# Kernel tuning notes

Hardware: AMD Instinct MI355X
Metric: run time of the kernel (lower is better)

## Reference

```python
import jax, jax.numpy as jnp
import numpy as np

B, L, C = 4, 1024, 768
H = 12
D = C // H  # head_dim = 64


def setup_inputs() -> dict:
    key = jax.random.key(0)
    k_x, k_qkv, k_pw, k_pb = jax.random.split(key, 4)
    x = jax.random.normal(k_x, (B, L, C), dtype=jnp.float32)
    # torch nn.Linear(C, 3C, bias=False): weight [3C, C]
    w_qkv = jax.random.normal(k_qkv, (3 * C, C), dtype=jnp.float32) * (1.0 / np.sqrt(C))
    # torch nn.Linear(C, C): weight [C, C], bias [C]
    w_proj = jax.random.normal(k_pw, (C, C), dtype=jnp.float32) * (1.0 / np.sqrt(C))
    b_proj = jax.random.normal(k_pb, (C,), dtype=jnp.float32) * 0.01
    return {"x": x, "w_qkv": w_qkv, "w_proj": w_proj, "b_proj": b_proj}


def reference(x, w_qkv, w_proj, b_proj):
    scale = D ** (-0.5)
    # qkv: [B, L, 3C] -> [3, B, H, L, D]
    qkv = jnp.einsum('blc,fc->blf', x, w_qkv)
    qkv = qkv.reshape(B, L, 3, H, D).transpose(2, 0, 3, 1, 4)
    q, k, v = qkv[0], qkv[1], qkv[2]
    # attention scores [B, H, L, L], materialized (returned by the module)
    attn = jnp.einsum('bhld,bhmd->bhlm', q, k) * scale
    attn_score = jax.nn.softmax(attn, axis=-1)
    # dropout_p = 0.0 -> identity
    out = jnp.einsum('bhlm,bhmd->bhld', attn_score, v)
    out = out.transpose(0, 2, 1, 3).reshape(B, L, C)
    out = jnp.einsum('blc,fc->blf', out, w_proj) + b_proj
    return (out, attn_score)
```

## Files before the change

kernel.cpp:

```cpp
#include <hip/hip_runtime.h>
#include <hip/hip_bf16.h>
#include <stdint.h>


typedef __attribute__((ext_vector_type(8))) short short8;
typedef __attribute__((ext_vector_type(4))) float floatx4;

#define MFMA16(A_, B_, C_) __builtin_amdgcn_mfma_f32_16x16x32_bf16((A_), (B_), (C_), 0, 0, 0)

__device__ __forceinline__ unsigned short f2bf(float f) {
  unsigned u = __builtin_bit_cast(unsigned, f);
  u += 0x7FFFu + ((u >> 16) & 1u);
  return (unsigned short)(u >> 16);
}
__device__ __forceinline__ float bf2f(unsigned short u) {
  return __builtin_bit_cast(float, (unsigned)u << 16);
}

__global__ __launch_bounds__(256) void cast3_kernel(const float* __restrict__ x,
                                                    const float* __restrict__ wq,
                                                    const float* __restrict__ wp,
                                                    unsigned short* __restrict__ dst) {
  const int NX = 3145728, NWQ = 1769472;
  int i = (blockIdx.x * 256 + threadIdx.x) * 4;
  const float* src;
  int off;
  if (i < NX) { src = x; off = i; }
  else if (i < NX + NWQ) { src = wq; off = i - NX; }
  else { src = wp; off = i - NX - NWQ; }
  float4 v = *(const float4*)(src + off);
  ushort4 o;
  o.x = f2bf(v.x); o.y = f2bf(v.y); o.z = f2bf(v.z); o.w = f2bf(v.w);
  *(ushort4*)(dst + i) = o;
}

template <int EPI>
__global__ __launch_bounds__(256) void gemm_bt(
    const unsigned short* __restrict__ A, const unsigned short* __restrict__ Bm,
    const float* __restrict__ bias,
    unsigned short* __restrict__ q_ws, unsigned short* __restrict__ k_ws,
    unsigned short* __restrict__ vt_ws, float* __restrict__ Cout,
    int M, int N, int K) {
  __shared__ __align__(16) unsigned short Al[128 * 32];
  __shared__ __align__(16) unsigned short Bl[128 * 32];
  const int tid = threadIdx.x;
  const int lane = tid & 63, wave = tid >> 6;
  const int q = lane >> 4, lm = lane & 15;
  const int wm = wave >> 1, wn = wave & 1;
  const int m0 = blockIdx.y * 128, n0 = blockIdx.x * 128;

  floatx4 acc[4][4];
#pragma unroll
  for (int i = 0; i < 4; ++i)
#pragma unroll
    for (int j = 0; j < 4; ++j) acc[i][j] = (floatx4){0.f, 0.f, 0.f, 0.f};

  for (int k0 = 0; k0 < K; k0 += 32) {
#pragma unroll
    for (int it = 0; it < 2; ++it) {
      int idx = tid + it * 256;
      int row = idx >> 2, ch = idx & 3;
      const unsigned short* ga = A + (size_t)(m0 + row) * K + k0 + ch * 8;
      const unsigned short* gb = Bm + (size_t)(n0 + row) * K + k0 + ch * 8;
      __builtin_amdgcn_global_load_lds(
          (const __attribute__((address_space(1))) unsigned int*)ga,
          (__attribute__((address_space(3))) unsigned int*)(Al + idx * 8), 16, 0, 0);
      __builtin_amdgcn_global_load_lds(
          (const __attribute__((address_space(1))) unsigned int*)gb,
          (__attribute__((address_space(3))) unsigned int*)(Bl + idx * 8), 16, 0, 0);
    }
    __syncthreads();
    short8 af[4], bfr[4];
#pragma unroll
    for (int t = 0; t < 4; ++t) {
      af[t] = *(const short8*)(Al + (wm * 64 + t * 16 + lm) * 32 + q * 8);
      bfr[t] = *(const short8*)(Bl + (wn * 64 + t * 16 + lm) * 32 + q * 8);
    }
#pragma unroll
    for (int i = 0; i < 4; ++i)
#pragma unroll
      for (int j = 0; j < 4; ++j) acc[i][j] = MFMA16(af[i], bfr[j], acc[i][j]);
    __syncthreads();
  }

  if (EPI == 0) {
#pragma unroll
    for (int i = 0; i < 4; ++i) {
      int mb = m0 + wm * 64 + i * 16 + q * 4;
#pragma unroll
      for (int j = 0; j < 4; ++j) {
        int n = n0 + wn * 64 + j * 16 + lm;
        int which = n / 768;
        int r = n - which * 768;
        int h = r >> 6, d = r & 63;
        if (which == 2) {
          int b = mb >> 10, l = mb & 1023;
          ushort4 pk;
          pk.x = f2bf(acc[i][j][0]);
          pk.y = f2bf(acc[i][j][1]);
          pk.z = f2bf(acc[i][j][2]);
          pk.w = f2bf(acc[i][j][3]);
          *(ushort4*)(vt_ws + (size_t)((b * 12 + h) * 64 + d) * 1024 + l) = pk;
        } else {
          unsigned short* dst = (which == 0) ? q_ws : k_ws;
          float sc = (which == 0) ? 0.125f : 1.0f;
#pragma unroll
          for (int rg = 0; rg < 4; ++rg) {
            int m = mb + rg;
            int b = m >> 10, l = m & 1023;
            dst[(size_t)((b * 12 + h) * 1024 + l) * 64 + d] = f2bf(acc[i][j][rg] * sc);
          }
        }
      }
    }
  } else {
#pragma unroll
    for (int i = 0; i < 4; ++i) {
      int mb = m0 + wm * 64 + i * 16 + q * 4;
#pragma unroll
      for (int j = 0; j < 4; ++j) {
        int n = n0 + wn * 64 + j * 16 + lm;
        float bv = bias[n];
#pragma unroll
        for (int rg = 0; rg < 4; ++rg) {
          int m = mb + rg;
          Cout[(size_t)m * N + n] = acc[i][j][rg] + bv;
        }
      }
    }
  }
}

__global__ __launch_bounds__(256) void attn_mfma(
    const unsigned short* __restrict__ q_ws, const unsigned short* __restrict__ k_ws,
    const unsigned short* __restrict__ vt_ws, unsigned short* __restrict__ attn_o,
    float* __restrict__ out1) {
  constexpr int L = 1024, SW = 1032;
  __shared__ __align__(16) unsigned short S[16 * SW];
  __shared__ float stats[2][4][16];
  const int bh = blockIdx.y, b = bh / 12, h = bh % 12;
  const int l0 = blockIdx.x * 16;
  const int tid = threadIdx.x, lane = tid & 63, wave = tid >> 6;
  const int q = lane >> 4, lm = lane & 15;

  const size_t qk_base = (size_t)bh * L * 64;

  const unsigned short* qr = q_ws + qk_base + (size_t)(l0 + lm) * 64;
  short8 bq0 = *(const short8*)(qr + q * 8);
  short8 bq1 = *(const short8*)(qr + 32 + q * 8);

  floatx4 acc[16];
#pragma unroll
  for (int ct = 0; ct < 16; ++ct) {
    const unsigned short* kr = k_ws + qk_base + (size_t)((wave * 16 + ct) * 16 + lm) * 64;
    short8 a0 = *(const short8*)(kr + q * 8);
    short8 a1 = *(const short8*)(kr + 32 + q * 8);
    floatx4 c = (floatx4){0.f, 0.f, 0.f, 0.f};
    c = MFMA16(a0, bq0, c);
    c = MFMA16(a1, bq1, c);
    acc[ct] = c;
  }

  float mloc = -1e30f;
#pragma unroll
  for (int ct = 0; ct < 16; ++ct)
#pragma unroll
    for (int rg = 0; rg < 4; ++rg) mloc = fmaxf(mloc, acc[ct][rg]);
  mloc = fmaxf(mloc, __shfl_xor(mloc, 16));
  mloc = fmaxf(mloc, __shfl_xor(mloc, 32));
  if (lane < 16) stats[0][wave][lane] = mloc;
  __syncthreads();
  float m = fmaxf(fmaxf(stats[0][0][lm], stats[0][1][lm]),
                  fmaxf(stats[0][2][lm], stats[0][3][lm]));

  float ssum = 0.f;
#pragma unroll
  for (int ct = 0; ct < 16; ++ct) {
#pragma unroll
    for (int rg = 0; rg < 4; ++rg) {
      float e = exp2f((acc[ct][rg] - m) * 1.44269504f);
      acc[ct][rg] = e;
      ssum += e;
    }
  }
  ssum += __shfl_xor(ssum, 16);
  ssum += __shfl_xor(ssum, 32);
  if (lane < 16) stats[1][wave][lane] = ssum;
  __syncthreads();
  float sinv = 1.0f / (stats[1][0][lm] + stats[1][1][lm] + stats[1][2][lm] + stats[1][3][lm]);

  float* orow = out1 + (size_t)bh * L * L + (size_t)(l0 + lm) * L + wave * 256 + q * 4;
  unsigned short* srow = S + lm * SW + wave * 256 + q * 4;
#pragma unroll
  for (int ct = 0; ct < 16; ++ct) {
    float p0 = acc[ct][0] * sinv, p1 = acc[ct][1] * sinv;
    float p2 = acc[ct][2] * sinv, p3 = acc[ct][3] * sinv;
    ushort4 pk;
    pk.x = f2bf(p0); pk.y = f2bf(p1); pk.z = f2bf(p2); pk.w = f2bf(p3);
    *(ushort4*)(srow + ct * 16) = pk;
    float4 pv;
    pv.x = p0; pv.y = p1; pv.z = p2; pv.w = p3;
    *(float4*)(orow + ct * 16) = pv;
  }
  __syncthreads();

  {
    floatx4 pacc = (floatx4){0.f, 0.f, 0.f, 0.f};
    const unsigned short* vr = vt_ws + (size_t)(bh * 64 + wave * 16 + lm) * 1024;
#pragma unroll 4
    for (int ks = 0; ks < 32; ++ks) {
      short8 af = *(const short8*)(S + lm * SW + ks * 32 + q * 8);
      short8 bv = *(const short8*)(vr + ks * 32 + q * 8);
      pacc = MFMA16(af, bv, pacc);
    }
#pragma unroll
    for (int rg = 0; rg < 4; ++rg) {
      int row = q * 4 + rg;
      attn_o[(size_t)(b * 1024 + l0 + row) * 768 + h * 64 + wave * 16 + lm] = f2bf(pacc[rg]);
    }
  }
}

extern "C" void kernel_launch(void* const* d_in, const int* in_sizes, int n_in,
                              void* d_out, int out_size, void* d_ws, size_t ws_size,
                              hipStream_t stream) {
  const float* x      = (const float*)d_in[0];
  const float* w_qkv  = (const float*)d_in[1];
  const float* w_proj = (const float*)d_in[2];
  const float* b_proj = (const float*)d_in[3];

  float* out0 = (float*)d_out;
  float* out1 = out0 + (size_t)4096 * 768;

  const size_t NX = (size_t)4096 * 768;
  const size_t NWQ = (size_t)2304 * 768;
  const size_t NWP = (size_t)768 * 768;
  const size_t NQ = (size_t)48 * 1024 * 64;

  unsigned short* x_bf   = (unsigned short*)d_ws;
  unsigned short* wq_bf  = x_bf + NX;
  unsigned short* wp_bf  = wq_bf + NWQ;
  unsigned short* q_ws   = wp_bf + NWP;
  unsigned short* k_ws   = q_ws + NQ;
  unsigned short* vt_ws  = k_ws + NQ;
  unsigned short* attn_o = vt_ws + NQ;

  cast3_kernel<<<dim3((NX + NWQ + NWP) / 1024), dim3(256), 0, stream>>>(x, w_qkv, w_proj, x_bf);

  gemm_bt<0><<<dim3(2304 / 128, 4096 / 128), dim3(256), 0, stream>>>(
      x_bf, wq_bf, nullptr, q_ws, k_ws, vt_ws, nullptr, 4096, 2304, 768);

  attn_mfma<<<dim3(64, 48), dim3(256), 0, stream>>>(q_ws, k_ws, vt_ws, attn_o, out1);

  gemm_bt<1><<<dim3(768 / 128, 4096 / 128), dim3(256), 0, stream>>>(
      attn_o, wp_bf, b_proj, nullptr, nullptr, nullptr, out0, 4096, 768, 768);
}
```

Before: 359.3 us.

## Double-buffer GEMM LDS tiles and use narrower N tile for output projection

Measured after the change: 357.2 us. About the same (-0.6%).

```diff
diff --git a/kernel.cpp b/kernel.cpp
--- a/kernel.cpp
+++ b/kernel.cpp
@@ -34,53 +34,68 @@
   *(ushort4*)(dst + i) = o;
 }
 
-template <int EPI>
+template <int EPI, int BN>
 __global__ __launch_bounds__(256) void gemm_bt(
     const unsigned short* __restrict__ A, const unsigned short* __restrict__ Bm,
     const float* __restrict__ bias,
     unsigned short* __restrict__ q_ws, unsigned short* __restrict__ k_ws,
     unsigned short* __restrict__ vt_ws, float* __restrict__ Cout,
     int M, int N, int K) {
-  __shared__ __align__(16) unsigned short Al[128 * 32];
-  __shared__ __align__(16) unsigned short Bl[128 * 32];
+  constexpr int NJ = BN / 32;
+  constexpr int QN = BN / 2;
+  __shared__ __align__(16) unsigned short Al[2][128 * 32];
+  __shared__ __align__(16) unsigned short Bl[2][BN * 32];
   const int tid = threadIdx.x;
   const int lane = tid & 63, wave = tid >> 6;
   const int q = lane >> 4, lm = lane & 15;
   const int wm = wave >> 1, wn = wave & 1;
-  const int m0 = blockIdx.y * 128, n0 = blockIdx.x * 128;
-
-  floatx4 acc[4][4];
+  const int m0 = blockIdx.y * 128, n0 = blockIdx.x * BN;
+
+  floatx4 acc[4][NJ];
 #pragma unroll
   for (int i = 0; i < 4; ++i)
 #pragma unroll
-    for (int j = 0; j < 4; ++j) acc[i][j] = (floatx4){0.f, 0.f, 0.f, 0.f};
-
-  for (int k0 = 0; k0 < K; k0 += 32) {
+    for (int j = 0; j < NJ; ++j) acc[i][j] = (floatx4){0.f, 0.f, 0.f, 0.f};
+
+  auto stage = [&](int k0, int buf) {
 #pragma unroll
     for (int it = 0; it < 2; ++it) {
       int idx = tid + it * 256;
       int row = idx >> 2, ch = idx & 3;
       const unsigned short* ga = A + (size_t)(m0 + row) * K + k0 + ch * 8;
+      __builtin_amdgcn_global_load_lds(
+          (const __attribute__((address_space(1))) unsigned int*)ga,
+          (__attribute__((address_space(3))) unsigned int*)(&Al[buf][0] + idx * 8), 16, 0, 0);
+    }
+#pragma unroll
+    for (int it = 0; it < BN / 64; ++it) {
+      int idx = tid + it * 256;
+      int row = idx >> 2, ch = idx & 3;
       const unsigned short* gb = Bm + (size_t)(n0 + row) * K + k0 + ch * 8;
       __builtin_amdgcn_global_load_lds(
-          (const __attribute__((address_space(1))) unsigned int*)ga,
-          (__attribute__((address_space(3))) unsigned int*)(Al + idx * 8), 16, 0, 0);
-      __builtin_amdgcn_global_load_lds(
           (const __attribute__((address_space(1))) unsigned int*)gb,
-          (__attribute__((address_space(3))) unsigned int*)(Bl + idx * 8), 16, 0, 0);
-    }
+          (__attribute__((address_space(3))) unsigned int*)(&Bl[buf][0] + idx * 8), 16, 0, 0);
+    }
+  };
+
+  stage(0, 0);
+  __syncthreads();
+  int cur = 0;
+  for (int k0 = 0; k0 < K; k0 += 32) {
+    if (k0 + 32 < K) stage(k0 + 32, cur ^ 1);
+    short8 af[4], bfr[NJ];
+#pragma unroll
+    for (int t = 0; t < 4; ++t)
+      af[t] = *(const short8*)(&Al[cur][0] + (wm * 64 + t * 16 + lm) * 32 + q * 8);
+#pragma unroll
+    for (int t = 0; t < NJ; ++t)
+      bfr[t] = *(const short8*)(&Bl[cur][0] + (wn * QN + t * 16 + lm) * 32 + q * 8);
+#pragma unroll
+    for (int i = 0; i < 4; ++i)
+#pragma unroll
+      for (int j = 0; j < NJ; ++j) acc[i][j] = MFMA16(af[i], bfr[j], acc[i][j]);
     __syncthreads();
-    short8 af[4], bfr[4];
-#pragma unroll
-    for (int t = 0; t < 4; ++t) {
-      af[t] = *(const short8*)(Al + (wm * 64 + t * 16 + lm) * 32 + q * 8);
-      bfr[t] = *(const short8*)(Bl + (wn * 64 + t * 16 + lm) * 32 + q * 8);
-    }
-#pragma unroll
-    for (int i = 0; i < 4; ++i)
-#pragma unroll
-      for (int j = 0; j < 4; ++j) acc[i][j] = MFMA16(af[i], bfr[j], acc[i][j]);
-    __syncthreads();
+    cur ^= 1;
   }
 
   if (EPI == 0) {
@@ -88,8 +103,8 @@
     for (int i = 0; i < 4; ++i) {
       int mb = m0 + wm * 64 + i * 16 + q * 4;
 #pragma unroll
-      for (int j = 0; j < 4; ++j) {
-        int n = n0 + wn * 64 + j * 16 + lm;
+      for (int j = 0; j < NJ; ++j) {
+        int n = n0 + wn * QN + j * 16 + lm;
         int which = n / 768;
         int r = n - which * 768;
         int h = r >> 6, d = r & 63;
@@ -118,8 +133,8 @@
     for (int i = 0; i < 4; ++i) {
       int mb = m0 + wm * 64 + i * 16 + q * 4;
 #pragma unroll
-      for (int j = 0; j < 4; ++j) {
-        int n = n0 + wn * 64 + j * 16 + lm;
+      for (int j = 0; j < NJ; ++j) {
+        int n = n0 + wn * QN + j * 16 + lm;
         float bv = bias[n];
 #pragma unroll
         for (int rg = 0; rg < 4; ++rg) {
@@ -247,11 +262,11 @@
 
   cast3_kernel<<<dim3((NX + NWQ + NWP) / 1024), dim3(256), 0, stream>>>(x, w_qkv, w_proj, x_bf);
 
-  gemm_bt<0><<<dim3(2304 / 128, 4096 / 128), dim3(256), 0, stream>>>(
+  gemm_bt<0, 128><<<dim3(2304 / 128, 4096 / 128), dim3(256), 0, stream>>>(
       x_bf, wq_bf, nullptr, q_ws, k_ws, vt_ws, nullptr, 4096, 2304, 768);
 
   attn_mfma<<<dim3(64, 48), dim3(256), 0, stream>>>(q_ws, k_ws, vt_ws, attn_o, out1);
 
-  gemm_bt<1><<<dim3(768 / 128, 4096 / 128), dim3(256), 0, stream>>>(
+  gemm_bt<1, 64><<<dim3(768 / 64, 4096 / 128), dim3(256), 0, stream>>>(
       attn_o, wp_bf, b_proj, nullptr, nullptr, nullptr, out0, 4096, 768, 768);
 }
```
